# Optimization experiments

Hardware: AMD Instinct MI355X
Metric: run time of the kernel (lower is better)

Reference implementation:

```python
import jax, jax.numpy as jnp
import numpy as np

N, T, V = 32, 4096, 3
H = 512
CONNECTIVITY = 0.3
SPECTRAL_RADIUS = 0.99
NOISE_LEVEL = 0.01
N_DROP = 0


def _init_internal_weights(h, connectivity, spectral_radius):
    # Mirrors sparse.rand(...).todense(); nonzeros shifted by -0.5; normalized
    # so max |eigenvalue| == spectral_radius.
    rng = np.random.default_rng(0)
    w = rng.random((h, h)).astype(np.float32)
    mask = rng.random((h, h)) < connectivity
    w = np.where(mask, w - 0.5, 0.0).astype(np.float32)
    e_max = np.abs(np.linalg.eigvals(w)).max()
    w = w / (e_max / spectral_radius)
    return jnp.asarray(w, dtype=jnp.float32)


def setup_inputs() -> dict:
    key = jax.random.key(0)
    k_x, k_in, k_noise = jax.random.split(key, 3)
    X = jax.random.normal(k_x, (N, T, V), dtype=jnp.float32)
    # input weights: (2*bernoulli(U(0,1)) - 1) * 0.2  -> random signs * 0.2
    signs = 2.0 * jax.random.bernoulli(k_in, 0.5, (H, V)).astype(jnp.float32) - 1.0
    W_in = signs * 0.2
    W_int = _init_internal_weights(H, CONNECTIVITY, SPECTRAL_RADIUS)
    # per-step uniform noise, pre-drawn: (T, N, H)
    noise = jax.random.uniform(k_noise, (T, N, H), dtype=jnp.float32)
    return {"X": X, "W_in": W_in, "W_int": W_int, "noise": noise}


def reference(X, W_in, W_int, noise):
    # X: (N, T, V); W_in: (H, V); W_int: (H, H); noise: (T, N, H)
    n, t, _ = X.shape
    h = W_int.shape[0]
    # einsum('bij,kj->bki', X, W_in) indexed [:, :, t] == per-step input (N, H)
    inputs = jnp.einsum('btv,hv->tbh', X, W_in)  # (T, N, H)
    prev0 = jnp.full((n, h), 0.01, dtype=X.dtype)

    def step(prev, xs):
        x_t, n_t = xs
        s = jnp.tanh(prev @ W_int + x_t + n_t * NOISE_LEVEL)
        return s, s

    _, states = jax.lax.scan(step, prev0, (inputs, noise))  # (T, N, H)
    states = jnp.transpose(states, (1, 0, 2))  # (N, T, H)
    return states[:, N_DROP:, :]
```

## Files before the change

kernel.cpp:

```cpp
#include <hip/hip_runtime.h>
#include <stdint.h>

typedef _Float16 h2 __attribute__((ext_vector_type(2)));
typedef float    f4 __attribute__((ext_vector_type(4)));
typedef uint32_t u4 __attribute__((ext_vector_type(4)));

#if __has_builtin(__builtin_amdgcn_fdot2)
__device__ __forceinline__ float dot2(uint32_t a, uint32_t b, float c) {
    return __builtin_amdgcn_fdot2(__builtin_bit_cast(h2, a),
                                  __builtin_bit_cast(h2, b), c, false);
}
#else
__device__ __forceinline__ float dot2(uint32_t a, uint32_t b, float c) {
    h2 ha = __builtin_bit_cast(h2, a), hb = __builtin_bit_cast(h2, b);
    return c + (float)ha[0]*(float)hb[0] + (float)ha[1]*(float)hb[1];
}
#endif

__device__ __forceinline__ float fast_tanh(float z) {
    float e = __expf(2.0f * z);
    return 1.0f - 2.0f * __builtin_amdgcn_rcpf(e + 1.0f);
}

#define TT 4096
#define NB 32
#define HD 512
#define JL 12
#define JTOT 64
#define JR (JTOT - JL)

__global__ __attribute__((amdgpu_waves_per_eu(2, 2))) __launch_bounds__(512)
void esn_kernel(const float* __restrict__ X, const float* __restrict__ W_in,
                const float* __restrict__ W_int, const float* __restrict__ noise,
                float* __restrict__ out)
{
    __shared__ __align__(16) _Float16 s_buf[2][HD];
    __shared__ float pads[4][HD];
    __shared__ u4 wstash[8 * JL * 64];

    const int tid  = threadIdx.x;
    const int b    = blockIdx.x;
    const int w    = tid >> 6;
    const int l    = tid & 63;
    const int kg   = tid >> 7;
    const int colg = tid & 127;
    const int c0   = colg * 4;

    const float win0 = W_in[tid*3 + 0];
    const float win1 = W_in[tid*3 + 1];
    const float win2 = W_in[tid*3 + 2];

    uint32_t wreg[4][JR];
    {
        const f4* Wv = (const f4*)W_int;
        for (int j = 0; j < JL; ++j) {
            const int k = kg*128 + 2*j;
            f4 r0 = Wv[(size_t)k*128 + colg];
            f4 r1 = Wv[(size_t)(k+1)*128 + colg];
            u4 q;
            #pragma unroll
            for (int c = 0; c < 4; ++c) {
                h2 hw; hw[0] = (_Float16)r0[c]; hw[1] = (_Float16)r1[c];
                q[c] = __builtin_bit_cast(uint32_t, hw);
            }
            wstash[(w*JL + j)*64 + l] = q;
        }
        #pragma unroll
        for (int j = 0; j < JR; ++j) {
            const int k = kg*128 + 2*(JL + j);
            f4 r0 = Wv[(size_t)k*128 + colg];
            f4 r1 = Wv[(size_t)(k+1)*128 + colg];
            #pragma unroll
            for (int c = 0; c < 4; ++c) {
                h2 hw; hw[0] = (_Float16)r0[c]; hw[1] = (_Float16)r1[c];
                wreg[c][j] = __builtin_bit_cast(uint32_t, hw);
            }
        }
    }
    s_buf[0][tid] = (_Float16)0.01f;
    __syncthreads();

    const float* Xb   = X   + (size_t)b * TT * 3;
    float*       outb = out + (size_t)b * TT * HD;
    const size_t nb   = (size_t)b * HD + tid;

    int cur = 0;
    for (int t = 0; t < TT; ++t) {
        const float nz = noise[(size_t)t*(NB*HD) + nb];
        const float x0 = Xb[t*3 + 0];
        const float x1 = Xb[t*3 + 1];
        const float x2 = Xb[t*3 + 2];

        const u4* sv4 = (const u4*)((const uint32_t*)(&s_buf[cur][0]) + kg*64);
        float a0 = 0.f, a1 = 0.f, a2 = 0.f, a3 = 0.f;
        u4 sq;

        #pragma unroll
        for (int j = 0; j < JL; ++j) {
            if ((j & 3) == 0) sq = sv4[j >> 2];
            const uint32_t sv = sq[j & 3];
            u4 q = wstash[(w*JL + j)*64 + l];
            a0 = dot2(sv, q[0], a0);
            a1 = dot2(sv, q[1], a1);
            a2 = dot2(sv, q[2], a2);
            a3 = dot2(sv, q[3], a3);
        }
        #pragma unroll
        for (int j = 0; j < JR; ++j) {
            const int jg = JL + j;
            if ((jg & 3) == 0) sq = sv4[jg >> 2];
            const uint32_t sv = sq[jg & 3];
            a0 = dot2(sv, wreg[0][j], a0);
            a1 = dot2(sv, wreg[1][j], a1);
            a2 = dot2(sv, wreg[2][j], a2);
            a3 = dot2(sv, wreg[3][j], a3);
        }
        f4 pv; pv[0] = a0; pv[1] = a1; pv[2] = a2; pv[3] = a3;
        *(f4*)&pads[kg][c0] = pv;
        __syncthreads();

        float z = pads[0][tid] + pads[1][tid] + pads[2][tid] + pads[3][tid];
        z += win0*x0 + win1*x1 + win2*x2 + 0.01f*nz;
        const float s = fast_tanh(z);
        outb[(size_t)t*HD + tid] = s;
        s_buf[cur^1][tid] = (_Float16)s;
        __syncthreads();
        cur ^= 1;
    }
}

extern "C" void kernel_launch(void* const* d_in, const int* in_sizes, int n_in,
                              void* d_out, int out_size, void* d_ws, size_t ws_size,
                              hipStream_t stream)
{
    const float* X     = (const float*)d_in[0];
    const float* W_in  = (const float*)d_in[1];
    const float* W_int = (const float*)d_in[2];
    const float* noise = (const float*)d_in[3];
    float* out = (float*)d_out;

    esn_kernel<<<dim3(NB), dim3(512), 0, stream>>>(X, W_in, W_int, noise, out);
}
```

Measured before the change: 5.375 ms.

## Use 1024 threads with 8 k-groups and drop LDS weight stash

Doubles the block to 1024 threads, splitting the K dimension into 8 groups of 64 rows so each thread holds all of its W_int fp16 pairs in registers (32 per column). The LDS weight stash and its per-step reads go away, and the per-step dot-product chain per thread is halved. In exchange, the partial-sum reduction now reads 8 pads instead of 4, half the threads sit idle during the tanh/output phase, and barriers now cover 16 waves.

```diff
diff --git a/kernel.cpp b/kernel.cpp
--- a/kernel.cpp
+++ b/kernel.cpp
@@ -25,49 +25,36 @@
 #define TT 4096
 #define NB 32
 #define HD 512
-#define JL 12
-#define JTOT 64
-#define JR (JTOT - JL)
+#define KG 8
+#define JP 32
 
-__global__ __attribute__((amdgpu_waves_per_eu(2, 2))) __launch_bounds__(512)
+__global__ __attribute__((amdgpu_waves_per_eu(4, 4))) __launch_bounds__(1024)
 void esn_kernel(const float* __restrict__ X, const float* __restrict__ W_in,
                 const float* __restrict__ W_int, const float* __restrict__ noise,
                 float* __restrict__ out)
 {
     __shared__ __align__(16) _Float16 s_buf[2][HD];
-    __shared__ float pads[4][HD];
-    __shared__ u4 wstash[8 * JL * 64];
+    __shared__ float pads[KG][HD];
 
     const int tid  = threadIdx.x;
     const int b    = blockIdx.x;
-    const int w    = tid >> 6;
-    const int l    = tid & 63;
     const int kg   = tid >> 7;
     const int colg = tid & 127;
     const int c0   = colg * 4;
 
-    const float win0 = W_in[tid*3 + 0];
-    const float win1 = W_in[tid*3 + 1];
-    const float win2 = W_in[tid*3 + 2];
+    float win0 = 0.f, win1 = 0.f, win2 = 0.f;
+    if (tid < HD) {
+        win0 = W_in[tid*3 + 0];
+        win1 = W_in[tid*3 + 1];
+        win2 = W_in[tid*3 + 2];
+    }
 
-    uint32_t wreg[4][JR];
+    uint32_t wreg[4][JP];
     {
         const f4* Wv = (const f4*)W_int;
-        for (int j = 0; j < JL; ++j) {
-            const int k = kg*128 + 2*j;
-            f4 r0 = Wv[(size_t)k*128 + colg];
-            f4 r1 = Wv[(size_t)(k+1)*128 + colg];
-            u4 q;
-            #pragma unroll
-            for (int c = 0; c < 4; ++c) {
-                h2 hw; hw[0] = (_Float16)r0[c]; hw[1] = (_Float16)r1[c];
-                q[c] = __builtin_bit_cast(uint32_t, hw);
-            }
-            wstash[(w*JL + j)*64 + l] = q;
-        }
         #pragma unroll
-        for (int j = 0; j < JR; ++j) {
-            const int k = kg*128 + 2*(JL + j);
+        for (int j = 0; j < JP; ++j) {
+            const int k = kg*64 + 2*j;
             f4 r0 = Wv[(size_t)k*128 + colg];
             f4 r1 = Wv[(size_t)(k+1)*128 + colg];
             #pragma unroll
@@ -77,39 +64,30 @@
             }
         }
     }
-    s_buf[0][tid] = (_Float16)0.01f;
+    if (tid < HD) s_buf[0][tid] = (_Float16)0.01f;
     __syncthreads();
 
     const float* Xb   = X   + (size_t)b * TT * 3;
     float*       outb = out + (size_t)b * TT * HD;
-    const size_t nb   = (size_t)b * HD + tid;
 
     int cur = 0;
     for (int t = 0; t < TT; ++t) {
-        const float nz = noise[(size_t)t*(NB*HD) + nb];
-        const float x0 = Xb[t*3 + 0];
-        const float x1 = Xb[t*3 + 1];
-        const float x2 = Xb[t*3 + 2];
+        float nz = 0.f, x0 = 0.f, x1 = 0.f, x2 = 0.f;
+        if (tid < HD) {
+            nz = noise[((size_t)t*NB + b)*HD + tid];
+            x0 = Xb[t*3 + 0];
+            x1 = Xb[t*3 + 1];
+            x2 = Xb[t*3 + 2];
+        }
 
-        const u4* sv4 = (const u4*)((const uint32_t*)(&s_buf[cur][0]) + kg*64);
+        const u4* sv4 = (const u4*)(&s_buf[cur][0]);
         float a0 = 0.f, a1 = 0.f, a2 = 0.f, a3 = 0.f;
         u4 sq;
 
         #pragma unroll
-        for (int j = 0; j < JL; ++j) {
-            if ((j & 3) == 0) sq = sv4[j >> 2];
+        for (int j = 0; j < JP; ++j) {
+            if ((j & 3) == 0) sq = sv4[kg*8 + (j >> 2)];
             const uint32_t sv = sq[j & 3];
-            u4 q = wstash[(w*JL + j)*64 + l];
-            a0 = dot2(sv, q[0], a0);
-            a1 = dot2(sv, q[1], a1);
-            a2 = dot2(sv, q[2], a2);
-            a3 = dot2(sv, q[3], a3);
-        }
-        #pragma unroll
-        for (int j = 0; j < JR; ++j) {
-            const int jg = JL + j;
-            if ((jg & 3) == 0) sq = sv4[jg >> 2];
-            const uint32_t sv = sq[jg & 3];
             a0 = dot2(sv, wreg[0][j], a0);
             a1 = dot2(sv, wreg[1][j], a1);
             a2 = dot2(sv, wreg[2][j], a2);
@@ -119,11 +97,15 @@
         *(f4*)&pads[kg][c0] = pv;
         __syncthreads();
 
-        float z = pads[0][tid] + pads[1][tid] + pads[2][tid] + pads[3][tid];
-        z += win0*x0 + win1*x1 + win2*x2 + 0.01f*nz;
-        const float s = fast_tanh(z);
-        outb[(size_t)t*HD + tid] = s;
-        s_buf[cur^1][tid] = (_Float16)s;
+        if (tid < HD) {
+            float z = 0.f;
+            #pragma unroll
+            for (int k = 0; k < KG; ++k) z += pads[k][tid];
+            z += win0*x0 + win1*x1 + win2*x2 + 0.01f*nz;
+            const float s = fast_tanh(z);
+            outb[(size_t)t*HD + tid] = s;
+            s_buf[cur^1][tid] = (_Float16)s;
+        }
         __syncthreads();
         cur ^= 1;
     }
@@ -139,5 +121,5 @@
     const float* noise = (const float*)d_in[3];
     float* out = (float*)d_out;
 
-    esn_kernel<<<dim3(NB), dim3(512), 0, stream>>>(X, W_in, W_int, noise, out);
+    esn_kernel<<<dim3(NB), dim3(1024), 0, stream>>>(X, W_in, W_int, noise, out);
 }
```

Result: slower. 15.06 ms (+180.2%).
